# Kernel tuning notes

Hardware: AMD Instinct MI355X
Metric: run time of the kernel (lower is better)

The kernel has to match this reference:

```python
import jax, jax.numpy as jnp
import numpy as np

D = 256; H = 8; L = 4; K = 4; AS = 2; HD = D // H
KK = K * K
LEVEL_SHAPES = [(128, 128), (64, 64), (32, 32), (16, 16)]


def _kernel_indices():
    # kernel_size=4 (even): linspace(-1.5, 1.5, 4); stack [j, i] then / K
    idx = jnp.linspace(-1.5, 1.5, K)
    ii, jj = jnp.meshgrid(idx, idx, indexing='ij')
    return jnp.stack([jj, ii], axis=-1).reshape(-1, 2) / K  # (KK, 2)


def _bilinear(vf, g, Hl, Wl):
    # vf: (b, H, Hl*Wl, HD) per-level value; g: (b, l1, H, KK, 2) in [0,1]
    # grid_sample semantics, align_corners=False, zero padding
    b, l1, h, kk, _ = g.shape
    x = g[..., 0] * Wl - 0.5
    y = g[..., 1] * Hl - 0.5
    x0 = jnp.floor(x)
    y0 = jnp.floor(y)
    acc = None
    for dx, dy in ((0, 0), (1, 0), (0, 1), (1, 1)):
        xi = x0 + dx
        yi = y0 + dy
        w = (1.0 - jnp.abs(x - xi)) * (1.0 - jnp.abs(y - yi))
        valid = (xi >= 0) & (xi < Wl) & (yi >= 0) & (yi < Hl)
        idx = (jnp.clip(yi, 0, Hl - 1) * Wl + jnp.clip(xi, 0, Wl - 1)).astype(jnp.int32)
        idx = idx.transpose(0, 2, 1, 3).reshape(b, h, l1 * kk)
        gth = jnp.take_along_axis(vf, idx[..., None], axis=2)  # (b,H,l1*kk,HD)
        ww = (w * valid).transpose(0, 2, 1, 3).reshape(b, h, l1 * kk)
        c = gth * ww[..., None]
        acc = c if acc is None else acc + c
    return acc.reshape(b, h, l1, kk, HD).transpose(0, 2, 1, 3, 4)  # (b,l1,H,kk,HD)


def setup_inputs() -> dict:
    key = jax.random.key(0)
    ks = jax.random.split(key, 9)
    b, l1 = 4, 1024
    l2 = sum(h * w for h, w in LEVEL_SHAPES)  # 21760
    query = jax.random.normal(ks[0], (b, l1, D), jnp.float32)
    value = jax.random.normal(ks[1], (b, l2, D), jnp.float32)
    centers = jax.random.uniform(ks[2], (b, l1, 2), jnp.float32)
    sizes = jax.random.uniform(ks[3], (b, l1, 2), jnp.float32) * 0.2 + 0.05
    ref_windows = jnp.concatenate([centers, sizes], axis=-1)  # (b,l1,4) cx,cy,w,h
    s = 1.0 / np.sqrt(D)
    Wv = jax.random.normal(ks[4], (D, D), jnp.float32) * s
    bv = jnp.zeros((D,), jnp.float32)
    Wo = jax.random.normal(ks[5], (D, D), jnp.float32) * s
    bo = jnp.zeros((D,), jnp.float32)
    Wbox = jax.random.normal(ks[6], (L * H * 4, D), jnp.float32) * 0.01
    bbox = jax.random.uniform(ks[7], (H * L * 4,), jnp.float32)
    Wattn = jax.random.normal(ks[8], (H * L * AS * AS, D), jnp.float32) * s
    battn = jnp.zeros((H * L * AS * AS,), jnp.float32)
    v_shape = np.array(LEVEL_SHAPES, np.int64)
    starts = np.cumsum([0] + [h * w for h, w in LEVEL_SHAPES[:-1]])
    v_start_index = np.array(starts, np.int64)
    v_mask = jnp.zeros((b, l2), bool)
    return dict(query=query, value=value, ref_windows=ref_windows, Wv=Wv, bv=bv,
                Wo=Wo, bo=bo, Wbox=Wbox, bbox=bbox, Wattn=Wattn, battn=battn,
                v_shape=v_shape, v_start_index=v_start_index, v_mask=v_mask)


def reference(query, value, ref_windows, Wv, bv, Wo, bo, Wbox, bbox, Wattn, battn,
              v_shape, v_start_index, v_mask):
    b, l1, _ = query.shape
    l2 = value.shape[1]
    # value projection + padding mask
    v = value @ Wv.T + bv
    v = jnp.where(v_mask[..., None], 0.0, v).reshape(b, l2, H, HD)
    # where to attend: offset boxes -> sampling grid (normalizer=None branch)
    off = (query @ Wbox.T + bbox).reshape(b, l1, H, L, 4)
    refw = ref_windows[:, :, None, None, :]            # (b,l1,1,1,4)
    refsz = jnp.concatenate([refw[..., 2:4], refw[..., 2:4]], axis=-1)
    boxes = refw + off / 8.0 * refsz                   # (b,l1,H,L,4)
    center = boxes[..., None, :2]
    size = boxes[..., None, 2:]
    grid = center + _kernel_indices() * jax.nn.relu(size)  # (b,l1,H,L,KK,2)
    # attention weights (attn_size grid upsampled to kernel_size by repeat_interleave)
    aw = (query @ Wattn.T + battn).reshape(b, l1, H, L, AS, AS)
    nr = K // AS
    aw = jnp.repeat(jnp.repeat(aw, nr, axis=-1), nr, axis=-2)  # (b,l1,H,L,K,K)
    sw = jax.nn.softmax(aw.reshape(b, l1, H, -1), axis=-1).reshape(b, l1, H, L, KK)
    lw = jax.nn.softmax(aw, axis=3).reshape(b, l1, H, L, KK)
    out = jnp.zeros((b, l1, H, HD), query.dtype)
    mout = jnp.zeros((b, l1, H, HD), query.dtype)
    for li in range(L):
        Hl, Wl = int(v_shape[li, 0]), int(v_shape[li, 1])
        st = int(v_start_index[li])
        vf = v[:, st:st + Hl * Wl].transpose(0, 2, 1, 3)  # (b,H,Hl*Wl,HD)
        samp = _bilinear(vf, grid[:, :, :, li], Hl, Wl)   # (b,l1,H,KK,HD)
        out = out + jnp.einsum('bqhkd,bqhk->bqhd', samp, sw[:, :, :, li])
        mout = mout + jnp.einsum('bqhkd,bqhk->bqhd', samp, lw[:, :, :, li])
    out = out.reshape(b, l1, D) @ Wo.T + bo
    mout = mout.reshape(b, l1, D) @ Wo.T + bo
    return out, mout, aw
```

## Files before the change

kernel.cpp:

```cpp
#include <hip/hip_runtime.h>
#include <hip/hip_bf16.h>


typedef __attribute__((ext_vector_type(8))) short short8;
typedef __attribute__((ext_vector_type(4))) float f32x4;
typedef __attribute__((ext_vector_type(4))) unsigned int uint4v;

__device__ __forceinline__ unsigned short f2bf(float f) {
    unsigned int u = __float_as_uint(f);
    unsigned int r = u + 0x7FFFu + ((u >> 16) & 1u);
    return (unsigned short)(r >> 16);
}
__device__ __forceinline__ unsigned int pkbf(float a, float b) {
    __hip_bfloat162 h = __float22bfloat162_rn(float2{a, b});
    return *reinterpret_cast<unsigned int*>(&h);
}
__device__ __forceinline__ short8 pack2(float4 x, float4 y) {
    uint4v u;
    u[0] = pkbf(x.x, x.y); u[1] = pkbf(x.z, x.w);
    u[2] = pkbf(y.x, y.y); u[3] = pkbf(y.z, y.w);
    return __builtin_bit_cast(short8, u);
}

__device__ __forceinline__ void storeC(float* C, size_t i, float v) { C[i] = v; }
__device__ __forceinline__ void storeC(unsigned short* C, size_t i, float v) { C[i] = f2bf(v); }

#define LDA 56

template <typename OutT>
__device__ __forceinline__ void gemm_body(
    const float* __restrict__ A, const float* __restrict__ W,
    const float* __restrict__ bias, OutT* __restrict__ C,
    int N, int bm, int bn, unsigned short* As, unsigned short* Ws)
{
    const int tid  = threadIdx.x;
    const int lane = tid & 63;
    const int wave = tid >> 6;
    const int wm = (wave & 1) * 64;
    const int wn = (wave >> 1) * 64;
    const int lr = tid >> 1;
    const int lh = (tid & 1) * 16;
    const int kg = lane >> 4;
    const int lm = lane & 15;

    f32x4 acc[4][4];
#pragma unroll
    for (int i = 0; i < 4; ++i)
#pragma unroll
        for (int j = 0; j < 4; ++j) {
            acc[i][j][0] = 0.f; acc[i][j][1] = 0.f;
            acc[i][j][2] = 0.f; acc[i][j][3] = 0.f;
        }

    const float* Ap = A + (size_t)(bm + lr) * 256 + lh;
    const float* Wp = W + (size_t)(bn + lr) * 256 + lh;
    unsigned short* Asp = &As[lr * LDA + lh];
    unsigned short* Wsp = &Ws[lr * LDA + lh];

    for (int k0 = 0; k0 < 256; k0 += 32) {
        float4 a0 = *(const float4*)(Ap + k0);
        float4 a1 = *(const float4*)(Ap + k0 + 4);
        float4 a2 = *(const float4*)(Ap + k0 + 8);
        float4 a3 = *(const float4*)(Ap + k0 + 12);
        float4 w0 = *(const float4*)(Wp + k0);
        float4 w1 = *(const float4*)(Wp + k0 + 4);
        float4 w2 = *(const float4*)(Wp + k0 + 8);
        float4 w3 = *(const float4*)(Wp + k0 + 12);
        __syncthreads();
        *(short8*)(Asp)     = pack2(a0, a1);
        *(short8*)(Asp + 8) = pack2(a2, a3);
        *(short8*)(Wsp)     = pack2(w0, w1);
        *(short8*)(Wsp + 8) = pack2(w2, w3);
        __syncthreads();
        short8 af[4], bfr[4];
#pragma unroll
        for (int i = 0; i < 4; ++i)
            af[i] = *(const short8*)&As[(wm + i * 16 + lm) * LDA + kg * 8];
#pragma unroll
        for (int j = 0; j < 4; ++j)
            bfr[j] = *(const short8*)&Ws[(wn + j * 16 + lm) * LDA + kg * 8];
#pragma unroll
        for (int i = 0; i < 4; ++i)
#pragma unroll
            for (int j = 0; j < 4; ++j)
                acc[i][j] = __builtin_amdgcn_mfma_f32_16x16x32_bf16(
                    af[i], bfr[j], acc[i][j], 0, 0, 0);
    }

#pragma unroll
    for (int j = 0; j < 4; ++j) {
        int col = bn + wn + j * 16 + lm;
        float bcol = bias[col];
#pragma unroll
        for (int i = 0; i < 4; ++i) {
#pragma unroll
            for (int r = 0; r < 4; ++r) {
                int row = bm + wm + i * 16 + kg * 4 + r;
                storeC(C, (size_t)row * N + col, acc[i][j][r] + bcol);
            }
        }
    }
}

__global__ __launch_bounds__(256) void gemm_vq_kernel(
    const float* __restrict__ value, const float* __restrict__ Wv,
    const float* __restrict__ bv, unsigned short* __restrict__ v,
    const float* __restrict__ query,
    const float* __restrict__ Wbox, const float* __restrict__ bbox, float* __restrict__ off,
    const float* __restrict__ Wattn, const float* __restrict__ battn, float* __restrict__ awr)
{
    __shared__ __align__(16) unsigned short As[128 * LDA];
    __shared__ __align__(16) unsigned short Ws[128 * LDA];
    const int x = blockIdx.x;
    if (x < 1360) {
        gemm_body<unsigned short>(value, Wv, bv, v, 256,
                                  (x >> 1) * 128, (x & 1) * 128, As, Ws);
    } else {
        const int idx = x - 1360;
        const int bm = (idx & 31) * 128;
        if (idx < 32) gemm_body<float>(query, Wbox, bbox, off, 128, bm, 0, As, Ws);
        else          gemm_body<float>(query, Wattn, battn, awr, 128, bm, 0, As, Ws);
    }
}

__global__ __launch_bounds__(256) void gemm_f_kernel(
    const float* __restrict__ A, const float* __restrict__ W,
    const float* __restrict__ bias, float* __restrict__ C, int N)
{
    __shared__ __align__(16) unsigned short As[128 * LDA];
    __shared__ __align__(16) unsigned short Ws[128 * LDA];
    gemm_body<float>(A, W, bias, C, N, blockIdx.x * 128, blockIdx.y * 128, As, Ws);
}

__global__ __launch_bounds__(256) void sample_kernel(
    const unsigned short* __restrict__ v, const float* __restrict__ off,
    const float* __restrict__ awr, const float* __restrict__ refw,
    float* __restrict__ aw_out, float* __restrict__ acc)
{
    const int x  = blockIdx.x;
    const int bq = ((x & 3) << 10) | (x >> 2);
    const int b  = bq >> 10;
    const int t  = threadIdx.x;

    __shared__ float ref4[4];
    __shared__ float awl[128];
    __shared__ float bxs[128];
    __shared__ float swl[512];
    __shared__ float lwl[512];
    __shared__ int4  tp[16 * 129];

    if (t < 4)   ref4[t] = refw[bq * 4 + t];
    if (t < 128) awl[t] = awr[(size_t)bq * 128 + t];
    __syncthreads();

    if (t < 128) {
        float o = off[(size_t)bq * 128 + t];
        int comp = t & 3;
        float r0 = ref4[0], r1 = ref4[1], r2 = ref4[2], r3 = ref4[3];
        float bx;
        if (comp == 0)      bx = r0 + o * 0.125f * r2;
        else if (comp == 1) bx = r1 + o * 0.125f * r3;
        else if (comp == 2) bx = r2 + o * 0.125f * r2;
        else                bx = r3 + o * 0.125f * r3;
        bxs[t] = bx;

        const int h = t >> 4, r = t & 15;
        float a = awl[t];
        float m = a;
#pragma unroll
        for (int s = 1; s < 16; s <<= 1) m = fmaxf(m, __shfl_xor(m, s, 16));
        float se = expf(a - m);
#pragma unroll
        for (int s = 1; s < 16; s <<= 1) se += __shfl_xor(se, s, 16);
        const float inv_s = 1.0f / (4.0f * se);

        float* awq = aw_out + (size_t)bq * 512 + h * 64;
#pragma unroll
        for (int j = 0; j < 4; ++j) {
            int eidx = r * 4 + j;
            int l  = eidx >> 4;
            int ky = (eidx >> 2) & 3;
            int kx = eidx & 3;
            int pos = (ky >> 1) * 2 + (kx >> 1);
            float raw = awl[h * 16 + l * 4 + pos];
            swl[h * 64 + eidx] = expf(raw - m) * inv_s;
            int base = h * 16 + pos;
            float m2 = awl[base];
#pragma unroll
            for (int li = 1; li < 4; ++li) m2 = fmaxf(m2, awl[base + li * 4]);
            float s2 = 0.f;
#pragma unroll
            for (int li = 0; li < 4; ++li) s2 += expf(awl[base + li * 4] - m2);
            lwl[h * 64 + eidx] = expf(raw - m2) / s2;
            awq[eidx] = raw;
        }
    }
    __syncthreads();

    const int STs_[4] = {0, 16384, 20480, 21504};
    for (int e = t; e < 512; e += 256) {
        int eh = e >> 6, rem = e & 63, l = rem >> 4, kk = rem & 15;
        const float* bx = &bxs[eh * 16 + l * 4];
        float cx = bx[0], cy = bx[1];
        float bw = fmaxf(bx[2], 0.f), bh = fmaxf(bx[3], 0.f);
        float kx = -0.375f + 0.25f * (float)(kk & 3);
        float ky = -0.375f + 0.25f * (float)(kk >> 2);
        int Wl = 128 >> l;
        float xg = (cx + kx * bw) * (float)Wl - 0.5f;
        float yg = (cy + ky * bh) * (float)Wl - 0.5f;
        float x0f = floorf(xg), y0f = floorf(yg);
        int x0 = (int)x0f, y0 = (int)y0f;
        float fx = xg - x0f, fy = yg - y0f;
        float sww = swl[e], lww = lwl[e];
        int rowbase = b * 21760 + STs_[l];
        int seg = e >> 5;
        int4* dst = &tp[seg * 129 + (e & 31) * 4];
#pragma unroll
        for (int tap = 0; tap < 4; ++tap) {
            int dx = tap & 1, dy = tap >> 1;
            int xi = x0 + dx, yi = y0 + dy;
            float w = (dx ? fx : 1.f - fx) * (dy ? fy : 1.f - fy);
            if (xi < 0 || xi >= Wl || yi < 0 || yi >= Wl) w = 0.f;
            int xc = min(max(xi, 0), Wl - 1);
            int yc = min(max(yi, 0), Wl - 1);
            dst[tap] = int4{(rowbase + yc * Wl + xc) << 7,
                            __float_as_int(w * sww),
                            __float_as_int(w * lww), 0};
        }
    }
    __syncthreads();

    const int h = t >> 5;
    const int half = (t >> 4) & 1;
    const int c2 = t & 15;
    const unsigned int* v32 = (const unsigned int*)v;
    const int choff = h * 16 + c2;
    const int4* tps = &tp[(h * 2 + half) * 129];

    float ao0 = 0.f, ao1 = 0.f, am0 = 0.f, am1 = 0.f;
#pragma unroll 4
    for (int i = 0; i < 128; ++i) {
        int4 d = tps[i];
        unsigned int pv = v32[(size_t)(d.x + choff)];
        float v0 = __uint_as_float(pv << 16);
        float v1 = __uint_as_float(pv & 0xffff0000u);
        float wo = __int_as_float(d.y), wm = __int_as_float(d.z);
        ao0 = fmaf(v0, wo, ao0); ao1 = fmaf(v1, wo, ao1);
        am0 = fmaf(v0, wm, am0); am1 = fmaf(v1, wm, am1);
    }
    ao0 += __shfl_xor(ao0, 16); ao1 += __shfl_xor(ao1, 16);
    am0 += __shfl_xor(am0, 16); am1 += __shfl_xor(am1, 16);
    if (!half) {
        size_t base = (size_t)bq * 256 + h * 32 + 2 * c2;
        *(float2*)&acc[base]                       = float2{ao0, ao1};
        *(float2*)&acc[base + (size_t)4096 * 256]  = float2{am0, am1};
    }
}

extern "C" void kernel_launch(void* const* d_in, const int* in_sizes, int n_in,
                              void* d_out, int out_size, void* d_ws, size_t ws_size,
                              hipStream_t stream) {
    const float* query = (const float*)d_in[0];
    const float* value = (const float*)d_in[1];
    const float* refw  = (const float*)d_in[2];
    const float* Wv    = (const float*)d_in[3];
    const float* bv    = (const float*)d_in[4];
    const float* Wo    = (const float*)d_in[5];
    const float* bo    = (const float*)d_in[6];
    const float* Wbox  = (const float*)d_in[7];
    const float* bbox  = (const float*)d_in[8];
    const float* Wattn = (const float*)d_in[9];
    const float* battn = (const float*)d_in[10];

    float* out = (float*)d_out;
    float* aw_out = out + 2 * 1048576;

    unsigned short* v = (unsigned short*)d_ws;
    float* off = (float*)((char*)d_ws + 44564480);
    float* awr = off + 524288;
    float* acc = awr + 524288;

    gemm_vq_kernel<<<1424, 256, 0, stream>>>(value, Wv, bv, v,
                                             query, Wbox, bbox, off,
                                             Wattn, battn, awr);
    sample_kernel<<<4096, 256, 0, stream>>>(v, off, awr, refw, aw_out, acc);
    gemm_f_kernel<<<dim3(64, 2), 256, 0, stream>>>(acc, Wo, bo, out, 256);
}
```

Before: 275.8 us.

## Widen sample kernel to 512 threads with 8-byte value gathers

The sampling kernel now runs 512 threads per block. Each thread builds one sampling point's tap table instead of looping over two. In the gather phase each wave handles one head: 8 lanes cover 32 channels with uint2 (4 bf16) loads, and the 8 lane groups split the 128 taps by level and by alternating tap index. Partial sums are combined with a three-stage shuffle reduction, which replaces the two-way split plus single shuffle. The aim is fewer, wider gather loads and more parallelism per query, at the cost of extra shuffles and 8 accumulators per thread.

```diff
diff --git a/kernel.cpp b/kernel.cpp
--- a/kernel.cpp
+++ b/kernel.cpp
@@ -132,7 +132,7 @@
     gemm_body<float>(A, W, bias, C, N, blockIdx.x * 128, blockIdx.y * 128, As, Ws);
 }
 
-__global__ __launch_bounds__(256) void sample_kernel(
+__global__ __launch_bounds__(512, 8) void sample_kernel(
     const unsigned short* __restrict__ v, const float* __restrict__ off,
     const float* __restrict__ awr, const float* __restrict__ refw,
     float* __restrict__ aw_out, float* __restrict__ acc)
@@ -147,7 +147,7 @@
     __shared__ float bxs[128];
     __shared__ float swl[512];
     __shared__ float lwl[512];
-    __shared__ int4  tp[16 * 129];
+    __shared__ int4  tp[32 * 66];
 
     if (t < 4)   ref4[t] = refw[bq * 4 + t];
     if (t < 128) awl[t] = awr[(size_t)bq * 128 + t];
@@ -197,8 +197,9 @@
     }
     __syncthreads();
 
-    const int STs_[4] = {0, 16384, 20480, 21504};
-    for (int e = t; e < 512; e += 256) {
+    {
+        const int STs_[4] = {0, 16384, 20480, 21504};
+        int e = t;
         int eh = e >> 6, rem = e & 63, l = rem >> 4, kk = rem & 15;
         const float* bx = &bxs[eh * 16 + l * 4];
         float cx = bx[0], cy = bx[1];
@@ -213,8 +214,7 @@
         float fx = xg - x0f, fy = yg - y0f;
         float sww = swl[e], lww = lwl[e];
         int rowbase = b * 21760 + STs_[l];
-        int seg = e >> 5;
-        int4* dst = &tp[seg * 129 + (e & 31) * 4];
+        int4* dst = &tp[(eh * 4 + l) * 66 + kk * 4];
 #pragma unroll
         for (int tap = 0; tap < 4; ++tap) {
             int dx = tap & 1, dy = tap >> 1;
@@ -223,37 +223,49 @@
             if (xi < 0 || xi >= Wl || yi < 0 || yi >= Wl) w = 0.f;
             int xc = min(max(xi, 0), Wl - 1);
             int yc = min(max(yi, 0), Wl - 1);
-            dst[tap] = int4{(rowbase + yc * Wl + xc) << 7,
+            dst[tap] = int4{(rowbase + yc * Wl + xc) << 6,
                             __float_as_int(w * sww),
                             __float_as_int(w * lww), 0};
         }
     }
     __syncthreads();
 
-    const int h = t >> 5;
-    const int half = (t >> 4) & 1;
-    const int c2 = t & 15;
-    const unsigned int* v32 = (const unsigned int*)v;
-    const int choff = h * 16 + c2;
-    const int4* tps = &tp[(h * 2 + half) * 129];
-
-    float ao0 = 0.f, ao1 = 0.f, am0 = 0.f, am1 = 0.f;
+    const int h    = t >> 6;
+    const int lane = t & 63;
+    const int l    = (lane >> 4) & 3;
+    const int sub  = (lane >> 3) & 1;
+    const int cl   = lane & 7;
+    const uint2* vp = (const uint2*)v;
+    const int choff = h * 8 + cl;
+    const int4* sp = &tp[(h * 4 + l) * 66 + sub];
+
+    float a0 = 0.f, a1 = 0.f, a2 = 0.f, a3 = 0.f;
+    float m0 = 0.f, m1 = 0.f, m2 = 0.f, m3 = 0.f;
 #pragma unroll 4
-    for (int i = 0; i < 128; ++i) {
-        int4 d = tps[i];
-        unsigned int pv = v32[(size_t)(d.x + choff)];
-        float v0 = __uint_as_float(pv << 16);
-        float v1 = __uint_as_float(pv & 0xffff0000u);
+    for (int i = 0; i < 32; ++i) {
+        int4 d = sp[2 * i];
+        uint2 pv = vp[(size_t)(d.x + choff)];
+        float v0 = __uint_as_float(pv.x << 16);
+        float v1 = __uint_as_float(pv.x & 0xffff0000u);
+        float v2 = __uint_as_float(pv.y << 16);
+        float v3 = __uint_as_float(pv.y & 0xffff0000u);
         float wo = __int_as_float(d.y), wm = __int_as_float(d.z);
-        ao0 = fmaf(v0, wo, ao0); ao1 = fmaf(v1, wo, ao1);
-        am0 = fmaf(v0, wm, am0); am1 = fmaf(v1, wm, am1);
-    }
-    ao0 += __shfl_xor(ao0, 16); ao1 += __shfl_xor(ao1, 16);
-    am0 += __shfl_xor(am0, 16); am1 += __shfl_xor(am1, 16);
-    if (!half) {
-        size_t base = (size_t)bq * 256 + h * 32 + 2 * c2;
-        *(float2*)&acc[base]                       = float2{ao0, ao1};
-        *(float2*)&acc[base + (size_t)4096 * 256]  = float2{am0, am1};
+        a0 = fmaf(v0, wo, a0); a1 = fmaf(v1, wo, a1);
+        a2 = fmaf(v2, wo, a2); a3 = fmaf(v3, wo, a3);
+        m0 = fmaf(v0, wm, m0); m1 = fmaf(v1, wm, m1);
+        m2 = fmaf(v2, wm, m2); m3 = fmaf(v3, wm, m3);
+    }
+#pragma unroll
+    for (int s = 8; s <= 32; s <<= 1) {
+        a0 += __shfl_xor(a0, s); a1 += __shfl_xor(a1, s);
+        a2 += __shfl_xor(a2, s); a3 += __shfl_xor(a3, s);
+        m0 += __shfl_xor(m0, s); m1 += __shfl_xor(m1, s);
+        m2 += __shfl_xor(m2, s); m3 += __shfl_xor(m3, s);
+    }
+    if (lane < 8) {
+        size_t base = (size_t)bq * 256 + h * 32 + cl * 4;
+        *(float4*)&acc[base]                      = float4{a0, a1, a2, a3};
+        *(float4*)&acc[base + (size_t)4096 * 256] = float4{m0, m1, m2, m3};
     }
 }
 
@@ -283,6 +295,6 @@
     gemm_vq_kernel<<<1424, 256, 0, stream>>>(value, Wv, bv, v,
                                              query, Wbox, bbox, off,
                                              Wattn, battn, awr);
-    sample_kernel<<<4096, 256, 0, stream>>>(v, off, awr, refw, aw_out, acc);
+    sample_kernel<<<4096, 512, 0, stream>>>(v, off, awr, refw, aw_out, acc);
     gemm_f_kernel<<<dim3(64, 2), 256, 0, stream>>>(acc, Wo, bo, out, 256);
 }
```

Result: faster. 250.1 us (-9.3%).
